# Kernel tuning notes

Measured on AMD Instinct MI355X. Metric: run time of the kernel, lower is better.

## Reference

```python
import jax, jax.numpy as jnp
import numpy as np

MODEL_DIM = 1024
NUM_HEADS = 16
HEAD_DIM = MODEL_DIM // NUM_HEADS
ROPE_BASE = 10000.0


def apply_rope(x):
    # x: [B, H, S, D] -- rotate-half RoPE convention
    S, D = x.shape[-2], x.shape[-1]
    inv_freq = 1.0 / (ROPE_BASE ** (jnp.arange(0, D, 2, dtype=jnp.float32) / D))  # [D/2]
    t = jnp.arange(S, dtype=jnp.float32)
    freqs = t[:, None] * inv_freq[None, :]                  # [S, D/2]
    cos = jnp.concatenate([jnp.cos(freqs), jnp.cos(freqs)], axis=-1)  # [S, D]
    sin = jnp.concatenate([jnp.sin(freqs), jnp.sin(freqs)], axis=-1)
    x1, x2 = x[..., : D // 2], x[..., D // 2 :]
    rot = jnp.concatenate([-x2, x1], axis=-1)
    return x * cos + rot * sin


def setup_inputs() -> dict:
    key = jax.random.key(0)
    k1, k2, k3 = jax.random.split(key, 3)
    B, S, Dm = 4, 2048, MODEL_DIM
    std = 1.0 / np.sqrt(Dm)
    x = jax.random.normal(k1, (B, S, Dm), dtype=jnp.float32)
    w_qkv = jax.random.normal(k2, (Dm, 3 * Dm), dtype=jnp.float32) * std
    b_qkv = jnp.zeros((3 * Dm,), dtype=jnp.float32)
    w_out = jax.random.normal(k3, (Dm, Dm), dtype=jnp.float32) * std
    b_out = jnp.zeros((Dm,), dtype=jnp.float32)
    return {"x": x, "w_qkv": w_qkv, "b_qkv": b_qkv, "w_out": w_out, "b_out": b_out}


def reference(x, w_qkv, b_qkv, w_out, b_out):
    B, S, Dm = x.shape
    H, Dh = NUM_HEADS, HEAD_DIM
    scale = Dh ** -0.5
    qkv = x @ w_qkv + b_qkv                                  # [B, S, 3*Dm]
    qkv = qkv.reshape(B, S, 3, H, Dh).transpose(2, 0, 3, 1, 4)  # [3, B, H, S, Dh]
    q, k, v = qkv[0], qkv[1], qkv[2]
    q = apply_rope(q)
    k = apply_rope(k)
    scores = jnp.einsum("bhqd,bhkd->bhqk", q, k) * scale      # [B, H, S, S]
    causal = jnp.tril(jnp.ones((S, S), dtype=bool))
    scores = jnp.where(causal[None, None], scores, -jnp.inf)
    attn = jax.nn.softmax(scores, axis=-1)
    out = jnp.einsum("bhqk,bhkd->bhqd", attn, v)              # [B, H, S, Dh]
    out = out.transpose(0, 2, 1, 3).reshape(B, S, Dm)
    out = out @ w_out + b_out
    return out, attn
```

## Files before the change

kernel.cpp:

```cpp
#include <hip/hip_runtime.h>
#include <hip/hip_bf16.h>
#include <stdint.h>

typedef unsigned short u16;
typedef __attribute__((ext_vector_type(4))) float f32x4;
typedef __attribute__((ext_vector_type(8))) short s16x8;

#define SEQ 2048
#define NB 4
#define DM 1024
#define NHD 16
#define DH 64

__device__ __forceinline__ u16 f2bf(float f) {
  union { float f; uint32_t u; } v; v.f = f;
  return (u16)((v.u + 0x7FFFu + ((v.u >> 16) & 1u)) >> 16);
}
__device__ __forceinline__ float bf2f(u16 u) {
  union { uint32_t u; float f; } v; v.u = ((uint32_t)u) << 16;
  return v.f;
}
__device__ __forceinline__ void gload16(const u16* g, u16* l) {
  __builtin_amdgcn_global_load_lds((const __attribute__((address_space(1))) void*)g,
                                   (__attribute__((address_space(3))) void*)l, 16, 0, 0);
}

__device__ __forceinline__ void stage64x64_swz(const u16* gbase, long gstride,
                                               u16* lds, int tid) {
  int l = tid & 63, w = tid >> 6;
  int rsub = l >> 3;
  int srcElem = ((l & 7) ^ rsub) * 8;
  #pragma unroll
  for (int p = 0; p < 2; ++p) {
    int row0 = w * 16 + p * 8;
    gload16(gbase + (long)(row0 + rsub) * gstride + srcElem, lds + row0 * 64);
  }
}
__device__ __forceinline__ s16x8 frag_swz(const u16* lds, int row, int cb) {
  return *(const s16x8*)&lds[row * 64 + (cb ^ ((row & 7) << 3))];
}

__global__ __launch_bounds__(256) void k_cvt(const float* __restrict__ in,
                                             u16* __restrict__ out, int n4) {
  int idx = blockIdx.x * 256 + threadIdx.x;
  int stride = gridDim.x * 256;
  for (; idx < n4; idx += stride) {
    float4 v = ((const float4*)in)[idx];
    ushort4 o;
    o.x = f2bf(v.x); o.y = f2bf(v.y); o.z = f2bf(v.z); o.w = f2bf(v.w);
    ((ushort4*)out)[idx] = o;
  }
}

__global__ __launch_bounds__(256) void k_trig(float2* __restrict__ cs) {
  int t = blockIdx.x * 256 + threadIdx.x;
  int s = t >> 5, ih = t & 31;
  float fq = exp2f(-(float)ih * 0.4152410118609203f);
  float ang = (float)s * fq;
  cs[t] = make_float2(cosf(ang), sinf(ang));
}

__global__ __launch_bounds__(256) void k_tpose(const float* __restrict__ in,
                                               u16* __restrict__ out, int R, int C) {
  __shared__ u16 tile[64][65];
  int c0 = blockIdx.x * 64, r0 = blockIdx.y * 64;
  int tx = threadIdx.x & 63, ty = threadIdx.x >> 6;
  #pragma unroll
  for (int rr = ty; rr < 64; rr += 4)
    tile[rr][tx] = f2bf(in[(long)(r0 + rr) * C + c0 + tx]);
  __syncthreads();
  #pragma unroll
  for (int cc = ty; cc < 64; cc += 4)
    out[(long)(c0 + cc) * R + r0 + tx] = tile[tx][cc];
}

__global__ __launch_bounds__(256) void k_gemm_qkv(const u16* __restrict__ A,
                                                  const u16* __restrict__ Bt,
                                                  const float* __restrict__ bias,
                                                  const float2* __restrict__ cs,
                                                  u16* __restrict__ Qr,
                                                  u16* __restrict__ Kr,
                                                  u16* __restrict__ VtG) {
  const int K = DM;
  __shared__ u16 As[128 * 64];
  __shared__ u16 Bs[128 * 64];
  int tid = threadIdx.x, lane = tid & 63, wave = tid >> 6;
  int wm = (wave >> 1) * 64, wn = (wave & 1) * 64;
  long m0 = (long)blockIdx.y * 128, n0 = (long)blockIdx.x * 128;
  int lrow = lane & 15, lk8 = (lane >> 4) * 8;
  int srow = wave * 8 + (lane >> 3);
  int scol = (lane & 7) * 8;
  const u16* Ag = &A[(m0 + srow) * (long)K + scol];
  const u16* Bg = &Bt[(n0 + srow) * (long)K + scol];
  f32x4 acc[4][4] = {};
  for (int k0 = 0; k0 < K; k0 += 64) {
    __syncthreads();
    #pragma unroll
    for (int p = 0; p < 4; ++p) {
      gload16(Ag + (long)p * 32 * K + k0, &As[(p * 32 + wave * 8) * 64]);
      gload16(Bg + (long)p * 32 * K + k0, &Bs[(p * 32 + wave * 8) * 64]);
    }
    __syncthreads();
    #pragma unroll
    for (int h = 0; h < 2; ++h) {
      s16x8 af[4], bfr[4];
      #pragma unroll
      for (int t = 0; t < 4; ++t)
        af[t]  = *(const s16x8*)&As[(wm + t * 16 + lrow) * 64 + h * 32 + lk8];
      #pragma unroll
      for (int t = 0; t < 4; ++t)
        bfr[t] = *(const s16x8*)&Bs[(wn + t * 16 + lrow) * 64 + h * 32 + lk8];
      #pragma unroll
      for (int i = 0; i < 4; ++i)
        #pragma unroll
        for (int j = 0; j < 4; ++j)
          acc[i][j] = __builtin_amdgcn_mfma_f32_16x16x32_bf16(af[i], bfr[j], acc[i][j], 0, 0, 0);
    }
  }
  int coln = (int)(n0) + wn;
  int sec = coln >> 10;
  int hh = (coln & 1023) >> 6;
  int crow = (lane >> 4) * 4, ccol = lane & 15;
  int rowb = (int)m0 + wm;
  if (sec < 2) {
    u16* dst = (sec == 0) ? Qr : Kr;
    float sc = (sec == 0) ? 0.125f : 1.0f;
    #pragma unroll
    for (int j2 = 0; j2 < 2; ++j2) {
      int ih = j2 * 16 + ccol;
      float bv1 = bias[coln + j2 * 16 + ccol];
      float bv2 = bias[coln + j2 * 16 + ccol + 32];
      #pragma unroll
      for (int i = 0; i < 4; ++i) {
        #pragma unroll
        for (int r = 0; r < 4; ++r) {
          int row = rowb + i * 16 + crow + r;
          int b = row >> 11, s = row & 2047;
          float2 cv = cs[(s << 5) + ih];
          float v1 = acc[i][j2][r] + bv1;
          float v2 = acc[i][j2 + 2][r] + bv2;
          long ob = ((long)((b * NHD + hh) * SEQ + s)) * 64;
          dst[ob + ih]      = f2bf((v1 * cv.x - v2 * cv.y) * sc);
          dst[ob + ih + 32] = f2bf((v2 * cv.x + v1 * cv.y) * sc);
        }
      }
    }
  } else {
    #pragma unroll
    for (int i = 0; i < 4; ++i) {
      int row = rowb + i * 16 + crow;
      int b = row >> 11, sl = row & 2047;
      int jt = sl >> 6, sr = sl & 63;
      #pragma unroll
      for (int j = 0; j < 4; ++j) {
        int d = j * 16 + ccol;
        float bv = bias[coln + j * 16 + ccol];
        long idx = (((long)(b * NHD + hh) * 32 + jt) * 64 + d) * 64 + sr;
        ushort4 o;
        o.x = f2bf(acc[i][j][0] + bv); o.y = f2bf(acc[i][j][1] + bv);
        o.z = f2bf(acc[i][j][2] + bv); o.w = f2bf(acc[i][j][3] + bv);
        *(ushort4*)&VtG[idx] = o;
      }
    }
  }
}

template<int OUT_BF16>
__global__ __launch_bounds__(256) void k_gemm(const u16* __restrict__ A,
                                              const u16* __restrict__ Bt_g,
                                              const float* __restrict__ bias,
                                              void* __restrict__ Cout,
                                              int M, int N, int K) {
  __shared__ u16 As[128 * 64];
  __shared__ u16 Bs[128 * 64];
  int tid = threadIdx.x, lane = tid & 63, wave = tid >> 6;
  int wm = (wave >> 1) * 64, wn = (wave & 1) * 64;
  long m0 = (long)blockIdx.y * 128, n0 = (long)blockIdx.x * 128;
  int lrow = lane & 15, lk8 = (lane >> 4) * 8;
  int srow = wave * 8 + (lane >> 3);
  int scol = (lane & 7) * 8;
  const u16* Ag = &A[(m0 + srow) * (long)K + scol];
  const u16* Bg = &Bt_g[(n0 + srow) * (long)K + scol];
  f32x4 acc[4][4] = {};
  for (int k0 = 0; k0 < K; k0 += 64) {
    __syncthreads();
    #pragma unroll
    for (int p = 0; p < 4; ++p) {
      gload16(Ag + (long)p * 32 * K + k0, &As[(p * 32 + wave * 8) * 64]);
      gload16(Bg + (long)p * 32 * K + k0, &Bs[(p * 32 + wave * 8) * 64]);
    }
    __syncthreads();
    #pragma unroll
    for (int h = 0; h < 2; ++h) {
      s16x8 af[4], bfr[4];
      #pragma unroll
      for (int t = 0; t < 4; ++t)
        af[t]  = *(const s16x8*)&As[(wm + t * 16 + lrow) * 64 + h * 32 + lk8];
      #pragma unroll
      for (int t = 0; t < 4; ++t)
        bfr[t] = *(const s16x8*)&Bs[(wn + t * 16 + lrow) * 64 + h * 32 + lk8];
      #pragma unroll
      for (int i = 0; i < 4; ++i)
        #pragma unroll
        for (int j = 0; j < 4; ++j)
          acc[i][j] = __builtin_amdgcn_mfma_f32_16x16x32_bf16(af[i], bfr[j], acc[i][j], 0, 0, 0);
    }
  }
  int crow = (lane >> 4) * 4, ccol = lane & 15;
  #pragma unroll
  for (int i = 0; i < 4; ++i)
  #pragma unroll
  for (int j = 0; j < 4; ++j) {
    long col = n0 + wn + j * 16 + ccol;
    float bv = bias ? bias[col] : 0.f;
    #pragma unroll
    for (int r = 0; r < 4; ++r) {
      long row = m0 + wm + i * 16 + crow + r;
      float v = acc[i][j][r] + bv;
      if (OUT_BF16) ((u16*)Cout)[row * N + col] = f2bf(v);
      else          ((float*)Cout)[row * N + col] = v;
    }
  }
}

__global__ __launch_bounds__(256) void k_attn(const u16* __restrict__ Qr,
                                              const u16* __restrict__ Kr,
                                              const u16* __restrict__ VtG,
                                              float* __restrict__ attn,
                                              u16* __restrict__ ctx) {
  constexpr int LP = 72;
  __shared__ u16 Ks[64 * 64];
  __shared__ u16 Vs[64 * 64];
  __shared__ u16 Ps[4][16 * LP];
  int tid = threadIdx.x, lane = tid & 63, wave = tid >> 6;
  int wgid = blockIdx.x;
  int c = wgid & 7, t7 = wgid >> 3;
  int bh = c * 8 + (t7 >> 5);
  int qb = 31 - (t7 & 31);
  int q0 = qb * 64;
  int qw0 = q0 + wave * 16;
  int lrow = lane & 15, lg = lane >> 4, lk8 = (lane >> 4) * 8;
  const u16* Qb = Qr + (long)bh * SEQ * 64;
  const u16* Kb = Kr + (long)bh * SEQ * 64;
  const u16* Vtb = VtG + (long)bh * 32 * 4096;
  float* attn_bh = attn + (long)bh * SEQ * SEQ;

  s16x8 qf0 = *(const s16x8*)&Qb[(long)(qw0 + lrow) * 64 + lk8];
  s16x8 qf1 = *(const s16x8*)&Qb[(long)(qw0 + lrow) * 64 + 32 + lk8];

  int njt = qb + 1;

  float suml[4] = {0.f, 0.f, 0.f, 0.f};
  for (int jt = 0; jt < njt; ++jt) {
    __syncthreads();
    stage64x64_swz(Kb + (long)jt * 64 * 64, 64, Ks, tid);
    __syncthreads();
    int ctmax = (jt < njt - 1) ? 3 : wave;
    long k0 = (long)jt * 64;
    for (int ct = 0; ct <= ctmax; ++ct) {
      int row = ct * 16 + lrow;
      s16x8 kf0 = frag_swz(Ks, row, lk8);
      s16x8 kf1 = frag_swz(Ks, row, 32 + lk8);
      f32x4 sa = {0.f, 0.f, 0.f, 0.f};
      sa = __builtin_amdgcn_mfma_f32_16x16x32_bf16(qf0, kf0, sa, 0, 0, 0);
      sa = __builtin_amdgcn_mfma_f32_16x16x32_bf16(qf1, kf1, sa, 0, 0, 0);
      bool diag = (jt == njt - 1) && (ct == wave);
      int gcol = (int)k0 + ct * 16 + lrow;
      #pragma unroll
      for (int r = 0; r < 4; ++r) {
        int grow = qw0 + lg * 4 + r;
        float e = (!diag || gcol <= grow) ? __expf(sa[r]) : 0.f;
        suml[r] += e;
      }
    }
  }
  #pragma unroll
  for (int r = 0; r < 4; ++r) {
    float v = suml[r];
    v += __shfl_xor(v, 1, 16);
    v += __shfl_xor(v, 2, 16);
    v += __shfl_xor(v, 4, 16);
    v += __shfl_xor(v, 8, 16);
    suml[r] = 1.0f / v;
  }

  f32x4 oacc[4] = {};
  u16* ps = &Ps[wave][0];
  for (int jt = 0; jt < njt; ++jt) {
    __syncthreads();
    stage64x64_swz(Kb + (long)jt * 64 * 64, 64, Ks, tid);
    stage64x64_swz(Vtb + jt * 4096, 64, Vs, tid);
    __syncthreads();
    int ctmax = (jt < njt - 1) ? 3 : wave;
    long k0 = (long)jt * 64;
    #pragma unroll
    for (int ct = 0; ct < 4; ++ct) {
      if (ct <= ctmax) {
        int row = ct * 16 + lrow;
        s16x8 kf0 = frag_swz(Ks, row, lk8);
        s16x8 kf1 = frag_swz(Ks, row, 32 + lk8);
        f32x4 sa = {0.f, 0.f, 0.f, 0.f};
        sa = __builtin_amdgcn_mfma_f32_16x16x32_bf16(qf0, kf0, sa, 0, 0, 0);
        sa = __builtin_amdgcn_mfma_f32_16x16x32_bf16(qf1, kf1, sa, 0, 0, 0);
        bool diag = (jt == njt - 1) && (ct == wave);
        int gcol = (int)k0 + ct * 16 + lrow;
        #pragma unroll
        for (int r = 0; r < 4; ++r) {
          int grow = qw0 + lg * 4 + r;
          float e = (!diag || gcol <= grow) ? __expf(sa[r]) : 0.f;
          ps[(lg * 4 + r) * LP + ct * 16 + lrow] = f2bf(e * suml[r]);
        }
      } else {
        #pragma unroll
        for (int r = 0; r < 4; ++r)
          ps[(lg * 4 + r) * LP + ct * 16 + lrow] = 0;
      }
    }
    s16x8 pf0 = *(const s16x8*)&ps[lrow * LP + lk8];
    s16x8 pf1 = *(const s16x8*)&ps[lrow * LP + 32 + lk8];
    #pragma unroll
    for (int dt = 0; dt < 4; ++dt) {
      int row = dt * 16 + lrow;
      s16x8 vf0 = frag_swz(Vs, row, lk8);
      s16x8 vf1 = frag_swz(Vs, row, 32 + lk8);
      oacc[dt] = __builtin_amdgcn_mfma_f32_16x16x32_bf16(pf0, vf0, oacc[dt], 0, 0, 0);
      oacc[dt] = __builtin_amdgcn_mfma_f32_16x16x32_bf16(pf1, vf1, oacc[dt], 0, 0, 0);
    }
    #pragma unroll
    for (int it = 0; it < 4; ++it) {
      int prow = it * 4 + (lane >> 4);
      int c4 = lane & 15;
      ushort4 pv = *(const ushort4*)&ps[prow * LP + c4 * 4];
      f32x4 o;
      o.x = bf2f(pv.x); o.y = bf2f(pv.y); o.z = bf2f(pv.z); o.w = bf2f(pv.w);
      __builtin_nontemporal_store(o,
          (f32x4*)&attn_bh[(long)(qw0 + prow) * SEQ + k0 + c4 * 4]);
    }
  }

  {
    int cstart = q0 + 64;
    int zc4 = (SEQ - cstart) >> 2;
    f32x4 z = {0.f, 0.f, 0.f, 0.f};
    for (int row = 0; row < 64; ++row) {
      f32x4* dst = (f32x4*)&attn_bh[(long)(q0 + row) * SEQ + cstart];
      for (int cc = tid; cc < zc4; cc += 256)
        __builtin_nontemporal_store(z, &dst[cc]);
    }
  }

  int b = bh >> 4, h = bh & 15;
  #pragma unroll
  for (int dt = 0; dt < 4; ++dt)
  #pragma unroll
  for (int r = 0; r < 4; ++r) {
    long grow = qw0 + lg * 4 + r;
    long col = h * 64 + dt * 16 + lrow;
    ctx[((long)b * SEQ + grow) * DM + col] = f2bf(oacc[dt][r]);
  }
}

extern "C" void kernel_launch(void* const* d_in, const int* in_sizes, int n_in,
                              void* d_out, int out_size, void* d_ws, size_t ws_size,
                              hipStream_t stream) {
  const float* x     = (const float*)d_in[0];
  const float* w_qkv = (const float*)d_in[1];
  const float* b_qkv = (const float*)d_in[2];
  const float* w_out = (const float*)d_in[3];
  const float* b_out = (const float*)d_in[4];
  float* outp = (float*)d_out;
  float* attn = outp + (long)NB * SEQ * DM;

  char* ws = (char*)d_ws;
  u16* Qr  = (u16*)(ws);
  u16* Kr  = (u16*)(ws + 16777216L);
  u16* VtG = (u16*)(ws + 33554432L);
  u16* ctx = (u16*)(ws + 50331648L);
  u16* WoT = (u16*)(ws + 67108864L);

  u16*    Xb  = (u16*)attn;
  u16*    WqT = (u16*)((char*)attn + 16777216L);
  float2* cst = (float2*)((char*)attn + 23068672L);

  k_cvt<<<1024, 256, 0, stream>>>(x, Xb, (NB * SEQ * DM) / 4);
  k_trig<<<256, 256, 0, stream>>>(cst);
  k_tpose<<<dim3(3 * DM / 64, DM / 64), 256, 0, stream>>>(w_qkv, WqT, DM, 3 * DM);
  k_tpose<<<dim3(DM / 64, DM / 64), 256, 0, stream>>>(w_out, WoT, DM, DM);

  k_gemm_qkv<<<dim3(3 * DM / 128, NB * SEQ / 128), 256, 0, stream>>>(
      Xb, WqT, b_qkv, cst, Qr, Kr, VtG);

  k_attn<<<2048, 256, 0, stream>>>(Qr, Kr, VtG, attn, ctx);

  k_gemm<0><<<dim3(DM / 128, NB * SEQ / 128), 256, 0, stream>>>(
      ctx, WoT, b_out, outp, NB * SEQ, DM, DM);
}
```

Measured before the change: 376.5 us.

## Widen attention blocks to 128 query rows and double-buffer K in first pass

The attention kernel now runs 512-thread workgroups covering 128 query rows (8 waves), halving the grid so each staged K/V tile is shared by twice as many waves. The first (row-sum) pass ping-pongs K tiles between the Ks and Vs LDS buffers, prefetching the next tile while computing on the current one and using one barrier per iteration. Diagonal masking is reworked for the two 64-column tiles at the diagonal. Larger blocks cut global K/V traffic but reduce grid parallelism and may lower occupancy.

```diff
diff --git a/kernel.cpp b/kernel.cpp
--- a/kernel.cpp
+++ b/kernel.cpp
@@ -35,6 +35,14 @@
     int row0 = w * 16 + p * 8;
     gload16(gbase + (long)(row0 + rsub) * gstride + srcElem, lds + row0 * 64);
   }
+}
+__device__ __forceinline__ void stage64x64_swz8(const u16* gbase, long gstride,
+                                                u16* lds, int tid) {
+  int l = tid & 63, w = tid >> 6;
+  int rsub = l >> 3;
+  int srcElem = ((l & 7) ^ rsub) * 8;
+  int row0 = w * 8;
+  gload16(gbase + (long)(row0 + rsub) * gstride + srcElem, lds + row0 * 64);
 }
 __device__ __forceinline__ s16x8 frag_swz(const u16* lds, int row, int cb) {
   return *(const s16x8*)&lds[row * 64 + (cb ^ ((row & 7) << 3))];
@@ -223,7 +231,7 @@
   }
 }
 
-__global__ __launch_bounds__(256) void k_attn(const u16* __restrict__ Qr,
+__global__ __launch_bounds__(512) void k_attn(const u16* __restrict__ Qr,
                                               const u16* __restrict__ Kr,
                                               const u16* __restrict__ VtG,
                                               float* __restrict__ attn,
@@ -231,13 +239,13 @@
   constexpr int LP = 72;
   __shared__ u16 Ks[64 * 64];
   __shared__ u16 Vs[64 * 64];
-  __shared__ u16 Ps[4][16 * LP];
+  __shared__ u16 Ps[8][16 * LP];
   int tid = threadIdx.x, lane = tid & 63, wave = tid >> 6;
   int wgid = blockIdx.x;
   int c = wgid & 7, t7 = wgid >> 3;
-  int bh = c * 8 + (t7 >> 5);
-  int qb = 31 - (t7 & 31);
-  int q0 = qb * 64;
+  int bh = c * 8 + (t7 >> 4);
+  int qb = 15 - (t7 & 15);
+  int q0 = qb * 128;
   int qw0 = q0 + wave * 16;
   int lrow = lane & 15, lg = lane >> 4, lk8 = (lane >> 4) * 8;
   const u16* Qb = Qr + (long)bh * SEQ * 64;
@@ -248,23 +256,28 @@
   s16x8 qf0 = *(const s16x8*)&Qb[(long)(qw0 + lrow) * 64 + lk8];
   s16x8 qf1 = *(const s16x8*)&Qb[(long)(qw0 + lrow) * 64 + 32 + lk8];
 
-  int njt = qb + 1;
+  int njt = 2 * qb + 2;
 
   float suml[4] = {0.f, 0.f, 0.f, 0.f};
+  stage64x64_swz8(Kb, 64, Ks, tid);
+  __syncthreads();
   for (int jt = 0; jt < njt; ++jt) {
-    __syncthreads();
-    stage64x64_swz(Kb + (long)jt * 64 * 64, 64, Ks, tid);
-    __syncthreads();
-    int ctmax = (jt < njt - 1) ? 3 : wave;
+    const u16* cur = (jt & 1) ? Vs : Ks;
+    u16* nxt = (jt & 1) ? Ks : Vs;
+    if (jt + 1 < njt)
+      stage64x64_swz8(Kb + (long)(jt + 1) * 64 * 64, 64, nxt, tid);
+    int dt2 = jt - 2 * qb;
+    int wq = (dt2 < 0) ? 100 : (wave - 4 * dt2);
+    int ctmax = (wq < 3) ? wq : 3;
     long k0 = (long)jt * 64;
     for (int ct = 0; ct <= ctmax; ++ct) {
       int row = ct * 16 + lrow;
-      s16x8 kf0 = frag_swz(Ks, row, lk8);
-      s16x8 kf1 = frag_swz(Ks, row, 32 + lk8);
+      s16x8 kf0 = frag_swz(cur, row, lk8);
+      s16x8 kf1 = frag_swz(cur, row, 32 + lk8);
       f32x4 sa = {0.f, 0.f, 0.f, 0.f};
       sa = __builtin_amdgcn_mfma_f32_16x16x32_bf16(qf0, kf0, sa, 0, 0, 0);
       sa = __builtin_amdgcn_mfma_f32_16x16x32_bf16(qf1, kf1, sa, 0, 0, 0);
-      bool diag = (jt == njt - 1) && (ct == wave);
+      bool diag = (ct == wq);
       int gcol = (int)k0 + ct * 16 + lrow;
       #pragma unroll
       for (int r = 0; r < 4; ++r) {
@@ -273,6 +286,7 @@
         suml[r] += e;
       }
     }
+    __syncthreads();
   }
   #pragma unroll
   for (int r = 0; r < 4; ++r) {
@@ -288,10 +302,12 @@
   u16* ps = &Ps[wave][0];
   for (int jt = 0; jt < njt; ++jt) {
     __syncthreads();
-    stage64x64_swz(Kb + (long)jt * 64 * 64, 64, Ks, tid);
-    stage64x64_swz(Vtb + jt * 4096, 64, Vs, tid);
-    __syncthreads();
-    int ctmax = (jt < njt - 1) ? 3 : wave;
+    stage64x64_swz8(Kb + (long)jt * 64 * 64, 64, Ks, tid);
+    stage64x64_swz8(Vtb + jt * 4096, 64, Vs, tid);
+    __syncthreads();
+    int dt2 = jt - 2 * qb;
+    int wq = (dt2 < 0) ? 100 : (wave - 4 * dt2);
+    int ctmax = (wq < 3) ? wq : 3;
     long k0 = (long)jt * 64;
     #pragma unroll
     for (int ct = 0; ct < 4; ++ct) {
@@ -302,7 +318,7 @@
         f32x4 sa = {0.f, 0.f, 0.f, 0.f};
         sa = __builtin_amdgcn_mfma_f32_16x16x32_bf16(qf0, kf0, sa, 0, 0, 0);
         sa = __builtin_amdgcn_mfma_f32_16x16x32_bf16(qf1, kf1, sa, 0, 0, 0);
-        bool diag = (jt == njt - 1) && (ct == wave);
+        bool diag = (ct == wq);
         int gcol = (int)k0 + ct * 16 + lrow;
         #pragma unroll
         for (int r = 0; r < 4; ++r) {
@@ -339,12 +355,12 @@
   }
 
   {
-    int cstart = q0 + 64;
+    int cstart = q0 + 128;
     int zc4 = (SEQ - cstart) >> 2;
     f32x4 z = {0.f, 0.f, 0.f, 0.f};
-    for (int row = 0; row < 64; ++row) {
+    for (int row = 0; row < 128; ++row) {
       f32x4* dst = (f32x4*)&attn_bh[(long)(q0 + row) * SEQ + cstart];
-      for (int cc = tid; cc < zc4; cc += 256)
+      for (int cc = tid; cc < zc4; cc += 512)
         __builtin_nontemporal_store(z, &dst[cc]);
     }
   }
@@ -390,7 +406,7 @@
   k_gemm_qkv<<<dim3(3 * DM / 128, NB * SEQ / 128), 256, 0, stream>>>(
       Xb, WqT, b_qkv, cst, Qr, Kr, VtG);
 
-  k_attn<<<2048, 256, 0, stream>>>(Qr, Kr, VtG, attn, ctx);
+  k_attn<<<1024, 512, 0, stream>>>(Qr, Kr, VtG, attn, ctx);
 
   k_gemm<0><<<dim3(DM / 128, NB * SEQ / 128), 256, 0, stream>>>(
       ctx, WoT, b_out, outp, NB * SEQ, DM, DM);
```

New measurement: 376.6 us. About the same (+0.0%).
